# Optimization experiments

Measured on AMD Instinct MI355X. Metric: run time of the kernel, lower is better.

The kernel has to match this reference:

```python
import jax, jax.numpy as jnp
import numpy as np

B, T, IN, H, OUT = 64, 32, 256, 512, 256
M, W, R = 256, 64, 4            # nr_cells, cell_size, read_heads
NN_IN = IN + R * W              # 512
NN_OUT = H + R * W              # 768
IFACE = R * W + 3 * W + 5 * R + 3  # 471
CLIP = 20.0
DELTA = 1e-6


def setup_inputs():
    key = jax.random.key(0)
    ks = jax.random.split(key, 10)
    s = 0.05
    bound = float(np.sqrt(6.0 / (B * H + 2 * H)))  # xavier_uniform on (2,B,H)
    return {
        'x': jax.random.normal(ks[0], (B, T, IN), jnp.float32),
        'h0': jax.random.uniform(ks[1], (2, B, H), jnp.float32, -bound, bound),
        'Wih0': jax.random.normal(ks[2], (4 * H, NN_IN), jnp.float32) * s,
        'Whh0': jax.random.normal(ks[3], (4 * H, H), jnp.float32) * s,
        'bih0': jnp.zeros((4 * H,), jnp.float32),
        'bhh0': jnp.zeros((4 * H,), jnp.float32),
        'Wih1': jax.random.normal(ks[4], (4 * H, H), jnp.float32) * s,
        'Whh1': jax.random.normal(ks[5], (4 * H, H), jnp.float32) * s,
        'bih1': jnp.zeros((4 * H,), jnp.float32),
        'bhh1': jnp.zeros((4 * H,), jnp.float32),
        'Wif': jax.random.normal(ks[6], (IFACE, H), jnp.float32) * s,
        'bif': jnp.zeros((IFACE,), jnp.float32),
        'Wout': jax.random.normal(ks[7], (OUT, NN_OUT), jnp.float32) * s,
        'bout': jnp.zeros((OUT,), jnp.float32),
    }


def _lstm_cell(x, h, c, Wih, Whh, bih, bhh):
    g = x @ Wih.T + bih + h @ Whh.T + bhh
    i, f, gg, o = jnp.split(g, 4, axis=1)  # torch gate order i,f,g,o
    c = jax.nn.sigmoid(f) * c + jax.nn.sigmoid(i) * jnp.tanh(gg)
    h = jax.nn.sigmoid(o) * jnp.tanh(c)
    return h, c


def _content_weights(mem, keys, strengths):
    # mem: (b,M,W), keys: (b,K,W), strengths: (b,K) -> softmax over M
    mem_n = mem / (jnp.linalg.norm(mem, axis=2, keepdims=True) + DELTA)
    key_n = keys / (jnp.linalg.norm(keys, axis=2, keepdims=True) + DELTA)
    sim = jnp.einsum('bkw,bmw->bkm', key_n, mem_n)
    return jax.nn.softmax(sim * strengths[..., None], axis=2)


def _memory_step(xi, mem, link, prec, rw, ww, usage):
    b = xi.shape[0]
    o = 0
    rk = jnp.tanh(xi[:, :R * W].reshape(b, R, W)); o = R * W
    rs = jax.nn.softplus(xi[:, o:o + R]); o += R
    wk = jnp.tanh(xi[:, o:o + W]).reshape(b, 1, W); o += W
    ws = jax.nn.softplus(xi[:, o])[:, None]; o += 1
    ev = jax.nn.sigmoid(xi[:, o:o + W]); o += W
    wv = jnp.tanh(xi[:, o:o + W]); o += W
    fg = jax.nn.sigmoid(xi[:, o:o + R]); o += R
    ag = jax.nn.sigmoid(xi[:, o])[:, None]; o += 1
    wg = jax.nn.sigmoid(xi[:, o])[:, None]; o += 1
    rm = jax.nn.softmax(xi[:, o:o + 3 * R].reshape(b, R, 3), axis=2)

    # usage update (uses OLD read/write weights); single write head
    usage = usage + (1.0 - usage) * ww
    psi = jnp.prod(1.0 - fg[:, :, None] * rw, axis=1)
    usage = usage * psi

    # write content addressing on OLD memory
    wcw = _content_weights(mem, wk, ws)[:, 0]  # (b,M)

    # allocation by ascending sort of usage (exclusive cumprod)
    u = DELTA + (1.0 - DELTA) * usage
    phi = jnp.argsort(u, axis=1)
    sorted_u = jnp.take_along_axis(u, phi, axis=1)
    excl = jnp.cumprod(jnp.concatenate([jnp.ones((b, 1), u.dtype), sorted_u], axis=1), axis=1)[:, :-1]
    sorted_alloc = (1.0 - sorted_u) * excl
    alloc = jnp.take_along_axis(sorted_alloc, jnp.argsort(phi, axis=1), axis=1)

    ww = wg * (ag * alloc + (1.0 - ag) * wcw)  # (b,M)

    # erase + write
    mem = mem * (1.0 - ww[:, :, None] * ev[:, None, :]) + ww[:, :, None] * wv[:, None, :]

    # temporal link matrix + precedence
    prev_scale = 1.0 - ww[:, :, None] - ww[:, None, :]
    link = prev_scale * link + ww[:, :, None] * prec[:, None, :]
    link = link * (1.0 - jnp.eye(M, dtype=link.dtype))
    prec = (1.0 - ww.sum(axis=1, keepdims=True)) * prec + ww

    # read: directional weights use NEW link and OLD read weights; content uses NEW memory
    rcw = _content_weights(mem, rk, rs)               # (b,R,M)
    fwd = jnp.einsum('bij,brj->bri', link, rw)
    bwd = jnp.einsum('brj,bji->bri', rw, link)
    rw = rm[:, :, 0:1] * bwd + rm[:, :, 1:2] * fwd + rm[:, :, 2:3] * rcw
    rvec = jnp.einsum('brm,bmw->brw', rw, mem).reshape(b, R * W)
    return rvec, mem, link, prec, rw, ww, usage


def reference(x, h0, Wih0, Whh0, bih0, bhh0, Wih1, Whh1, bih1, bhh1, Wif, bif, Wout, bout):
    b = x.shape[0]
    lr0 = jnp.zeros((b, R * W), x.dtype)  # initial last_read; NOTE: source concatenates this
    # initial zero last_read to EVERY timestep's controller input (inputs built upfront)
    carry0 = (h0[0], h0[0], h0[1], h0[1],
              jnp.full((b, M, W), DELTA, x.dtype),   # memory
              jnp.zeros((b, M, M), x.dtype),          # link matrix
              jnp.zeros((b, M), x.dtype),             # precedence
              jnp.full((b, R, M), DELTA, x.dtype),    # read weights
              jnp.full((b, M), DELTA, x.dtype),       # write weights
              jnp.zeros((b, M), x.dtype))             # usage

    def step(carry, x_t):
        h0_, c0_, h1_, c1_, mem, link, prec, rw, ww, usage = carry
        inp = jnp.concatenate([x_t, lr0], axis=1)
        h0_, c0_ = _lstm_cell(inp, h0_, c0_, Wih0, Whh0, bih0, bhh0)
        h1_, c1_ = _lstm_cell(h0_, h1_, c1_, Wih1, Whh1, bih1, bhh1)
        out = jnp.clip(h1_, -CLIP, CLIP)
        xi = out @ Wif.T + bif
        rvec, mem, link, prec, rw, ww, usage = _memory_step(xi, mem, link, prec, rw, ww, usage)
        o_t = jnp.concatenate([out, rvec], axis=1)  # (b, NN_OUT)
        return (h0_, c0_, h1_, c1_, mem, link, prec, rw, ww, usage), o_t

    _, ys = jax.lax.scan(step, carry0, jnp.swapaxes(x, 0, 1))  # (T,b,NN_OUT)
    outputs = jnp.tanh(ys) @ Wout.T + bout  # Dropout(p=0) -> Tanh -> Linear
    return jnp.swapaxes(outputs, 0, 1)      # (b,T,OUT)
```

## Files before the change

kernel.cpp:

```cpp
#include <hip/hip_runtime.h>
#include <hip/hip_bf16.h>
#include <math.h>


typedef __bf16 bf16_t;
typedef __attribute__((ext_vector_type(8))) __bf16 bf16x8;
typedef __attribute__((ext_vector_type(4))) float f32x4;

#define B_    64
#define T_    32
#define IN_   256
#define H_    512
#define M_    256
#define W_    64
#define R_    4
#define IFACE_ 471
#define DELTA_ 1e-6f

#define OFF_H0SEQ  (0L)
#define SZ_H0SEQ   (32L*64*512*2)
#define OFF_OUTSEQ (OFF_H0SEQ + SZ_H0SEQ)
#define SZ_OUTSEQ  (32L*64*512*2)
#define OFF_H0BUF  (OFF_OUTSEQ + SZ_OUTSEQ)
#define SZ_HBUF    (2L*64*512*2)
#define OFF_H1BUF  (OFF_H0BUF + SZ_HBUF)
#define OFF_XI     (OFF_H1BUF + SZ_HBUF)
#define SZ_XI      (32L*64*480*4)
#define OFF_RVEC   (OFF_XI + SZ_XI)
#define SZ_RVEC    (32L*64*256*4)
#define OFF_YBF    (OFF_RVEC + SZ_RVEC)
#define SZ_YBF     (32L*64*768*2)
#define OFF_BAR    (OFF_YBF + SZ_YBF)
#define SZ_BAR     (256L)
#define OFF_XB     (OFF_BAR + SZ_BAR)
#define SZ_XB      (64L*32*256*2)
#define OFF_H0B    (OFF_XB + SZ_XB)
#define SZ_H0B     (2L*64*512*2)
#define OFF_W0     (OFF_H0B + SZ_H0B)
#define SZ_W       (2048L*512*2)
#define OFF_W1     (OFF_W0 + SZ_W)
#define OFF_W2     (OFF_W1 + SZ_W)
#define OFF_W3     (OFF_W2 + SZ_W)
#define OFF_WIF    (OFF_W3 + SZ_W)
#define SZ_WIF     (480L*512*2)
#define OFF_WOUTB  (OFF_WIF + SZ_WIF)
#define SZ_WOUTB   (256L*768*2)
#define OFF_BS0    (OFF_WOUTB + SZ_WOUTB)
#define SZ_BS      (2048L*4)
#define OFF_BS1    (OFF_BS0 + SZ_BS)
#define OFF_BIF    (OFF_BS1 + SZ_BS)
#define SZ_BIF     (2048L)
#define OFF_BOUTF  (OFF_BIF + SZ_BIF)
#define SZ_BOUTF   (1024L)
#define OFF_FLG    (OFF_BOUTF + SZ_BOUTF)
#define SZ_FLG     (4096L)

__device__ __forceinline__ float sigf(float x){ return 1.0f/(1.0f + expf(-x)); }
__device__ __forceinline__ float softplusf(float x){
  return fmaxf(x, 0.0f) + log1pf(expf(-fabsf(x)));
}
__device__ __forceinline__ float wred(float v){
  #pragma unroll
  for (int off = 32; off; off >>= 1) v += __shfl_xor(v, off, 64);
  return v;
}
__device__ __forceinline__ float ldin(const void* p, long i, int mf){
  return mf ? ((const float*)p)[i] : (float)((const bf16_t*)p)[i];
}

__device__ __forceinline__ void flagbar(unsigned* flg, int bid, unsigned tgt,
                                        int tid, int lane, int wv){
  __syncthreads();
  if (tid == 0)
    __hip_atomic_store(flg + (size_t)bid*16, tgt, __ATOMIC_RELEASE,
                       __HIP_MEMORY_SCOPE_AGENT);
  if (wv == 0){
    for (;;){
      unsigned f = __hip_atomic_load(flg + (size_t)lane*16, __ATOMIC_ACQUIRE,
                                     __HIP_MEMORY_SCOPE_AGENT);
      if (__all(f >= tgt)) break;
      __builtin_amdgcn_s_sleep(2);
    }
  }
  __syncthreads();
}

__global__ void k_detect(const unsigned short* __restrict__ x16,
                         int* __restrict__ flag, unsigned* __restrict__ bar,
                         unsigned* __restrict__ flg){
  __shared__ int cnt;
  if (threadIdx.x == 0){ cnt = 0; bar[0] = 0u; bar[1] = 0u; }
  for (int i = threadIdx.x; i < 1024; i += 256) flg[i] = 0u;
  __syncthreads();
  unsigned short u = x16[threadIdx.x * 2];
  int e = (u >> 7) & 0xFF;
  if (e >= 0x88) atomicAdd(&cnt, 1);
  __syncthreads();
  if (threadIdx.x == 0) *flag = (cnt > 16) ? 1 : 0;
}

__global__ void k_convert(const void* x, const void* h0, const void* Wih0,
                          const void* Whh0, const void* bih0, const void* bhh0,
                          const void* Wih1, const void* Whh1, const void* bih1,
                          const void* bhh1, const void* Wif, const void* bif,
                          const void* Wout, const void* bout,
                          bf16_t* __restrict__ xb, bf16_t* __restrict__ h0b,
                          bf16_t* __restrict__ h0buf, bf16_t* __restrict__ h1buf,
                          bf16_t* __restrict__ W0, bf16_t* __restrict__ W1,
                          bf16_t* __restrict__ W2, bf16_t* __restrict__ W3,
                          bf16_t* __restrict__ Wifp, bf16_t* __restrict__ Woutb,
                          float* __restrict__ bs0, float* __restrict__ bs1,
                          float* __restrict__ bifp, float* __restrict__ boutf,
                          const int* __restrict__ flag)
{
  const int mf = *flag;
  const long stride = (long)gridDim.x * blockDim.x;
  long i0 = (long)blockIdx.x * blockDim.x + threadIdx.x;
  switch (blockIdx.y){
  case 0: for (long i = i0; i < 64L*32*256; i += stride) xb[i] = (bf16_t)ldin(x, i, mf); break;
  case 1: for (long i = i0; i < 2L*64*512; i += stride){
            float v = ldin(h0, i, mf); bf16_t bb = (bf16_t)v; h0b[i] = bb;
            if (i < 64*512) h0buf[i] = bb; else h1buf[i - 64*512] = bb;
          } break;
  case 2: for (long i = i0; i < 2048L*512; i += stride) W0[i] = (bf16_t)ldin(Wih0, i, mf); break;
  case 3: for (long i = i0; i < 2048L*512; i += stride) W1[i] = (bf16_t)ldin(Whh0, i, mf); break;
  case 4: for (long i = i0; i < 2048L*512; i += stride) W2[i] = (bf16_t)ldin(Wih1, i, mf); break;
  case 5: for (long i = i0; i < 2048L*512; i += stride) W3[i] = (bf16_t)ldin(Whh1, i, mf); break;
  case 6: for (long i = i0; i < 480L*512; i += stride){
            long r = i >> 9;
            Wifp[i] = (r < IFACE_) ? (bf16_t)ldin(Wif, i, mf) : (bf16_t)0.0f;
          } break;
  case 7: for (long i = i0; i < 256L*768; i += stride) Woutb[i] = (bf16_t)ldin(Wout, i, mf); break;
  case 8:
    for (long i = i0; i < 2048; i += stride){
      bs0[i] = ldin(bih0, i, mf) + ldin(bhh0, i, mf);
      bs1[i] = ldin(bih1, i, mf) + ldin(bhh1, i, mf);
    }
    for (long i = i0; i < 480; i += stride) bifp[i] = (i < IFACE_) ? ldin(bif, i, mf) : 0.0f;
    for (long i = i0; i < 256; i += stride) boutf[i] = ldin(bout, i, mf);
    break;
  }
}

__device__ __forceinline__ void softmax256_wave(float* a, int lane){
  float v0=a[lane], v1=a[64+lane], v2=a[128+lane], v3=a[192+lane];
  float mx = fmaxf(fmaxf(v0,v1), fmaxf(v2,v3));
  #pragma unroll
  for (int off=32; off; off>>=1) mx = fmaxf(mx, __shfl_xor(mx, off, 64));
  v0=expf(v0-mx); v1=expf(v1-mx); v2=expf(v2-mx); v3=expf(v3-mx);
  float s = v0+v1+v2+v3;
  #pragma unroll
  for (int off=32; off; off>>=1) s += __shfl_xor(s, off, 64);
  float inv = 1.0f/s;
  a[lane]=v0*inv; a[64+lane]=v1*inv; a[128+lane]=v2*inv; a[192+lane]=v3*inv;
}

struct ProdShm {
  bf16_t wpool[66560];
  float  cst[64][16];
  float  bias[4][16];
};
struct ConsShm {
  float smem[256][65];
  float xib[480];
  float rkn4r[2][65][4];
  float wkn[64], ev_[64], wvv[64];
  float rs_[4], fg_[4], rm_[4][3];
  float wsS, agS, wgS, wwsumS;
  float invn[256], wcw[256];
  float usage[256], uu[256], su[256], scanA[256];
  int   rank_[256];
  float ww_[256], prec_[256];
  float rw_[4][256];
  float rw4[256][4];
  float fwd_[4][256], bwd_[4][256], rcw_[4][256];
  bf16_t rwb[4][264];
  bf16_t wwb[256], precb[256];
  float p2cT[2][264];
  float p5cT[5][2][264];
  float rvp[8][4][64];
};
union ShUnion { ProdShm p; ConsShm c; };

__global__ __launch_bounds__(512,2) void k_main(
    const bf16_t* __restrict__ xb, const bf16_t* __restrict__ h0b,
    const bf16_t* __restrict__ W0, const bf16_t* __restrict__ W1,
    const bf16_t* __restrict__ W2, const bf16_t* __restrict__ W3,
    const float* __restrict__ bs0, const float* __restrict__ bs1,
    const bf16_t* __restrict__ Wifp, const float* __restrict__ bifp,
    bf16_t* __restrict__ h0buf, bf16_t* __restrict__ h1buf,
    bf16_t* __restrict__ h0seq, bf16_t* __restrict__ outseq,
    float* __restrict__ XI, float* __restrict__ RVEC,
    unsigned* __restrict__ flg)
{
  __shared__ ShUnion sh;
  const int bid = blockIdx.x;
  const int tid = threadIdx.x, lane = tid & 63, wv = tid >> 6;
  const int m16 = lane & 15, q = lane >> 4;

  if (bid < 64){
    ProdShm& P = sh.p;
    const int layer = bid >> 5;
    const int u0 = (bid & 31) * 16;

    if (!layer){
      for (int i = tid; i < 64*32; i += 512){
        int rl = i >> 5, c8 = (i & 31)*8;
        int grow = (rl >> 4)*512 + u0 + (rl & 15);
        *(bf16x8*)&P.wpool[rl*264 + c8] = *(const bf16x8*)(W0 + (size_t)grow*512 + c8);
      }
      for (int i = tid; i < 64*64; i += 512){
        int rl = i >> 6, c8 = (i & 63)*8;
        int grow = (rl >> 4)*512 + u0 + (rl & 15);
        *(bf16x8*)&P.wpool[16896 + rl*520 + c8] = *(const bf16x8*)(W1 + (size_t)grow*512 + c8);
      }
    } else {
      for (int i = tid; i < 64*64; i += 512){
        int rl = i >> 6, c8 = (i & 63)*8;
        int grow = (rl >> 4)*512 + u0 + (rl & 15);
        *(bf16x8*)&P.wpool[rl*520 + c8]         = *(const bf16x8*)(W2 + (size_t)grow*512 + c8);
        *(bf16x8*)&P.wpool[33280 + rl*520 + c8] = *(const bf16x8*)(W3 + (size_t)grow*512 + c8);
      }
    }
    for (int i = tid; i < 64*16; i += 512){
      int b = i >> 4, n = i & 15;
      P.cst[b][n] = (float)h0b[layer*(64*512) + b*512 + u0 + n];
    }
    if (tid < 64){
      int G = tid >> 4, n = tid & 15;
      const float* bs = layer ? bs1 : bs0;
      P.bias[G][n] = bs[G*512 + u0 + n];
    }
    __syncthreads();

    bf16_t* hbuf = layer ? h1buf : h0buf;

    for (int ps = 0; ps <= 33; ++ps){
      if (wv < 4){
        const int t = layer ? (ps - 1) : ps;
        const bool active = layer ? (ps >= 1 && ps <= 32) : (ps < 32);
        if (active){
          const int p = t & 1;
          const bf16_t* hin = hbuf + p*(64*512);
          bf16_t* hout = hbuf + (p^1)*(64*512);
          const int b0 = wv * 16;

          f32x4 acc[4];
          #pragma unroll
          for (int G = 0; G < 4; ++G){ float bv = P.bias[G][m16]; acc[G] = (f32x4){bv,bv,bv,bv}; }

          if (!layer){
            #pragma unroll 2
            for (int kt = 0; kt < 8; ++kt){
              bf16x8 a = *(const bf16x8*)(xb + ((size_t)(b0+m16)*T_ + t)*IN_ + kt*32 + q*8);
              #pragma unroll
              for (int G = 0; G < 4; ++G)
                acc[G] = __builtin_amdgcn_mfma_f32_16x16x32_bf16(
                    a, *(const bf16x8*)&P.wpool[(G*16+m16)*264 + kt*32 + q*8], acc[G], 0, 0, 0);
            }
            #pragma unroll 4
            for (int kt = 0; kt < 16; ++kt){
              bf16x8 a = *(const bf16x8*)(hin + (b0+m16)*512 + kt*32 + q*8);
              #pragma unroll
              for (int G = 0; G < 4; ++G)
                acc[G] = __builtin_amdgcn_mfma_f32_16x16x32_bf16(
                    a, *(const bf16x8*)&P.wpool[16896 + (G*16+m16)*520 + kt*32 + q*8], acc[G], 0, 0, 0);
            }
          } else {
            #pragma unroll 4
            for (int kt = 0; kt < 16; ++kt){
              bf16x8 a = *(const bf16x8*)(h0seq + ((size_t)t*64 + b0+m16)*512 + kt*32 + q*8);
              #pragma unroll
              for (int G = 0; G < 4; ++G)
                acc[G] = __builtin_amdgcn_mfma_f32_16x16x32_bf16(
                    a, *(const bf16x8*)&P.wpool[(G*16+m16)*520 + kt*32 + q*8], acc[G], 0, 0, 0);
            }
            #pragma unroll 4
            for (int kt = 0; kt < 16; ++kt){
              bf16x8 a = *(const bf16x8*)(hin + (b0+m16)*512 + kt*32 + q*8);
              #pragma unroll
              for (int G = 0; G < 4; ++G)
                acc[G] = __builtin_amdgcn_mfma_f32_16x16x32_bf16(
                    a, *(const bf16x8*)&P.wpool[33280 + (G*16+m16)*520 + kt*32 + q*8], acc[G], 0, 0, 0);
            }
          }
          #pragma unroll
          for (int v = 0; v < 4; ++v){
            int b = b0 + q*4 + v;
            float gi = acc[0][v], gf = acc[1][v], gg = acc[2][v], go = acc[3][v];
            float c_ = sigf(gf)*P.cst[b][m16] + sigf(gi)*tanhf(gg);
            P.cst[b][m16] = c_;
            float h = sigf(go)*tanhf(c_);
            bf16_t hb = (bf16_t)h;
            hout[b*512 + u0 + m16] = hb;
            if (!layer) h0seq[((size_t)t*64 + b)*512 + u0 + m16] = hb;
            else        outseq[((size_t)t*64 + b)*512 + u0 + m16] = hb;
          }
        }
      } else if (ps >= 2 && bid < 30){
        const int t2 = ps - 2;
        const int b0 = (wv - 4) * 16;
        const int r = bid*16 + m16;
        float bv = bifp[r];
        f32x4 acc = {bv,bv,bv,bv};
        const bf16_t* arow = outseq + ((size_t)t2*64 + b0 + m16)*512 + q*8;
        const bf16_t* brow = Wifp + (size_t)r*512 + q*8;
        #pragma unroll 4
        for (int kt = 0; kt < 16; ++kt){
          acc = __builtin_amdgcn_mfma_f32_16x16x32_bf16(
              *(const bf16x8*)(arow + kt*32), *(const bf16x8*)(brow + kt*32), acc, 0, 0, 0);
        }
        #pragma unroll
        for (int v = 0; v < 4; ++v)
          XI[((size_t)t2*64 + b0 + q*4 + v)*480 + r] = acc[v];
      }
      flagbar(flg, bid, (unsigned)(ps + 1), tid, lane, wv);
    }
  } else {
    ConsShm& S = sh.c;
    const int b = bid - 64;
    const int quad = lane >> 4, li = lane & 15;

    bf16x8 rowL[2][8], colL[2][8];
    #pragma unroll
    for (int g = 0; g < 2; ++g)
      #pragma unroll
      for (int ch = 0; ch < 8; ++ch)
        #pragma unroll
        for (int z = 0; z < 8; ++z){ rowL[g][ch][z] = (bf16_t)0.0f; colL[g][ch][z] = (bf16_t)0.0f; }

    if (tid < 256){
      S.ww_[tid] = DELTA_; S.usage[tid] = 0.0f; S.prec_[tid] = 0.0f;
      S.invn[tid] = 1.0f/(sqrtf(64.0f*DELTA_*DELTA_) + DELTA_);
      S.wwb[tid] = (bf16_t)DELTA_; S.precb[tid] = (bf16_t)0.0f;
      #pragma unroll
      for (int r = 0; r < 4; ++r) S.rw_[r][tid] = DELTA_;
    }
    for (int i = tid; i < 4*264; i += 512) ((bf16_t*)S.rwb)[i] = (bf16_t)DELTA_;
    for (int i = tid; i < 256*65; i += 512) ((float*)S.smem)[i] = DELTA_;
    __syncthreads();

    const int mH = tid >> 1, q2 = tid & 1;

    for (int t = 0; t < 32; ++t){
      { const unsigned tgt = (unsigned)(t + 3);
        if (wv == 0){
          for (;;){
            unsigned f = __hip_atomic_load(flg + (size_t)lane*16, __ATOMIC_ACQUIRE,
                                           __HIP_MEMORY_SCOPE_AGENT);
            if (__all(f >= tgt)) break;
            __builtin_amdgcn_s_sleep(2);
          }
        }
        __syncthreads();
      }
      if (tid < IFACE_) S.xib[tid] = XI[((size_t)t*64 + b)*480 + tid];
      __syncthreads();

      if (wv < 4){
        float v = tanhf(S.xib[wv*64 + lane]);
        float s = wred(v*v);
        float vn = v/(sqrtf(s) + DELTA_);
        S.rkn4r[0][lane][wv] = vn; S.rkn4r[1][lane][wv] = vn;
      } else if (wv == 4){
        float v = tanhf(S.xib[260 + lane]);
        float s = wred(v*v);
        S.wkn[lane] = v/(sqrtf(s) + DELTA_);
      } else if (wv == 5){ S.ev_[lane] = sigf(S.xib[325 + lane]);
      } else if (wv == 6){ S.wvv[lane] = tanhf(S.xib[389 + lane]);
      } else {
        if (lane < 4)        S.rs_[lane] = softplusf(S.xib[256 + lane]);
        else if (lane == 4)  S.wsS = softplusf(S.xib[324]);
        else if (lane < 9)   S.fg_[lane-5] = sigf(S.xib[453 + (lane-5)]);
        else if (lane == 9)  S.agS = sigf(S.xib[457]);
        else if (lane == 10) S.wgS = sigf(S.xib[458]);
        else if (lane >= 16 && lane < 20){
          int r = lane - 16;
          float a0 = S.xib[459+r*3], a1 = S.xib[459+r*3+1], a2 = S.xib[459+r*3+2];
          float mx = fmaxf(a0, fmaxf(a1, a2));
          float e0 = expf(a0-mx), e1 = expf(a1-mx), e2 = expf(a2-mx);
          float s = e0+e1+e2;
          S.rm_[r][0]=e0/s; S.rm_[r][1]=e1/s; S.rm_[r][2]=e2/s;
        }
      }
      __syncthreads();

      if (tid < 256){
        int m = tid;
        float us = S.usage[m] + (1.0f - S.usage[m])*S.ww_[m];
        float psi = (1.0f - S.fg_[0]*S.rw_[0][m]) * (1.0f - S.fg_[1]*S.rw_[1][m])
                  * (1.0f - S.fg_[2]*S.rw_[2][m]) * (1.0f - S.fg_[3]*S.rw_[3][m]);
        us *= psi;
        S.usage[m] = us;
        S.uu[m] = DELTA_ + (1.0f - DELTA_)*us;
      }
      { float acc = 0.0f;
        #pragma unroll
        for (int it = 0; it < 32; ++it){
          int w = q2*32 + it;
          acc += S.smem[mH][w] * S.wkn[w];
        }
        S.p2cT[q2][mH] = acc; }
      __syncthreads();

      if (wv == 0){
        #pragma unroll
        for (int z = 0; z < 4; ++z){
          int m = z*64 + lane;
          S.wcw[m] = S.wsS * (S.p2cT[0][m] + S.p2cT[1][m]) * S.invn[m];
        }
        softmax256_wave(S.wcw, lane);
      } else if (tid >= 256){
        const int i = tid - 256;
        const float ui = S.uu[i];
        int cnt = 0;
        #pragma unroll 8
        for (int k = 0; k < 64; ++k){
          f32x4 u4 = *(const f32x4*)&S.uu[k*4];
          #pragma unroll
          for (int z = 0; z < 4; ++z){
            int j = k*4 + z; float uj = u4[z];
            cnt += (uj < ui || (uj == ui && j < i)) ? 1 : 0;
          }
        }
        S.rank_[i] = cnt;
        S.su[cnt] = ui;
      }
      __syncthreads();

      if (wv == 0){
        int base = lane*4;
        float v0 = S.su[base], v1 = S.su[base+1], v2 = S.su[base+2];
        float p1 = v0*v1, p2 = p1*v2, p3 = p2*S.su[base+3];
        float sc = p3;
        #pragma unroll
        for (int off = 1; off < 64; off <<= 1){
          float n = __shfl_up(sc, off, 64);
          if (lane >= off) sc *= n;
        }
        float exch = __shfl_up(sc, 1, 64);
        if (lane == 0) exch = 1.0f;
        S.scanA[base] = exch; S.scanA[base+1] = exch*v0;
        S.scanA[base+2] = exch*p1; S.scanA[base+3] = exch*p2;
      }
      __syncthreads();

      { const int m = mH;
        float al = (1.0f - S.uu[m]) * S.scanA[S.rank_[m]];
        float wm = S.wgS*(S.agS*al + (1.0f - S.agS)*S.wcw[m]);
        if (q2 == 0){ S.ww_[m] = wm; S.wwb[m] = (bf16_t)wm; }
        float s2 = 0.0f, sr0 = 0.0f, sr1 = 0.0f, sr2 = 0.0f, sr3 = 0.0f;
        #pragma unroll
        for (int it = 0; it < 32; ++it){
          int w = q2*32 + it;
          float mn = S.smem[m][w]*(1.0f - wm*S.ev_[w]) + wm*S.wvv[w];
          S.smem[m][w] = mn;
          s2 += mn*mn;
          f32x4 rk = *(const f32x4*)&S.rkn4r[q2][w][0];
          sr0 += mn*rk[0]; sr1 += mn*rk[1]; sr2 += mn*rk[2]; sr3 += mn*rk[3];
        }
        S.p5cT[0][q2][m] = s2;
        S.p5cT[1][q2][m] = sr0; S.p5cT[2][q2][m] = sr1;
        S.p5cT[3][q2][m] = sr2; S.p5cT[4][q2][m] = sr3; }
      __syncthreads();

      if (tid < 256){
        int m = tid;
        float s2 = S.p5cT[0][0][m] + S.p5cT[0][1][m];
        float inv = 1.0f/(sqrtf(s2) + DELTA_);
        S.invn[m] = inv;
        #pragma unroll
        for (int r = 0; r < 4; ++r){
          float sr = S.p5cT[r+1][0][m] + S.p5cT[r+1][1][m];
          S.rcw_[r][m] = S.rs_[r]*sr*inv;
        }
      } else if (wv == 4){
        float s = wred(S.ww_[lane] + S.ww_[64+lane] + S.ww_[128+lane] + S.ww_[192+lane]);
        if (lane == 0) S.wwsumS = s;
      }
      __syncthreads();

      { float wown[2], pown[2], alpha[2];
        #pragma unroll
        for (int g = 0; g < 2; ++g){
          int o = wv*32 + g*16 + li;
          wown[g] = (float)S.wwb[o]; pown[g] = (float)S.precb[o];
          alpha[g] = 1.0f - wown[g];
        }
        f32x4 facc[2] = {{0,0,0,0},{0,0,0,0}}, bacc[2] = {{0,0,0,0},{0,0,0,0}};
        #pragma unroll
        for (int ch = 0; ch < 8; ++ch){
          const int cbase = ch*32 + quad*8;
          bf16x8 rwf = *(const bf16x8*)&S.rwb[li & 3][cbase];
          bf16x8 wwv = *(const bf16x8*)&S.wwb[cbase];
          bf16x8 pcv = *(const bf16x8*)&S.precb[cbase];
          float wcf[8], pcf[8];
          #pragma unroll
          for (int jj = 0; jj < 8; ++jj){ wcf[jj] = (float)wwv[jj]; pcf[jj] = (float)pcv[jj]; }
          #pragma unroll
          for (int g = 0; g < 2; ++g){
            const int o = wv*32 + g*16 + li;
            bf16x8 rl = rowL[g][ch];
            bf16x8 cl = colL[g][ch];
            #pragma unroll
            for (int jj = 0; jj < 8; ++jj){
              const int c = cbase + jj;
              float s = alpha[g] - wcf[jj];
              float vr = s*(float)rl[jj] + wown[g]*pcf[jj];
              float vc = s*(float)cl[jj] + wcf[jj]*pown[g];
              if (c == o){ vr = 0.0f; vc = 0.0f; }
              rl[jj] = (bf16_t)vr;
              cl[jj] = (bf16_t)vc;
            }
            rowL[g][ch] = rl; colL[g][ch] = cl;
            facc[g] = __builtin_amdgcn_mfma_f32_16x16x32_bf16(rl, rwf, facc[g], 0, 0, 0);
            bacc[g] = __builtin_amdgcn_mfma_f32_16x16x32_bf16(rwf, cl, bacc[g], 0, 0, 0);
          }
        }
        #pragma unroll
        for (int g = 0; g < 2; ++g){
          if (li < 4){
            #pragma unroll
            for (int z = 0; z < 4; ++z) S.fwd_[li][wv*32 + g*16 + quad*4 + z] = facc[g][z];
          }
          if (quad == 0){
            #pragma unroll
            for (int z = 0; z < 4; ++z) S.bwd_[z][wv*32 + g*16 + li] = bacc[g][z];
          }
        }
      }
      __syncthreads();

      if (wv < 4) softmax256_wave(S.rcw_[wv], lane);
      else {
        int m = tid - 256;
        float p = (1.0f - S.wwsumS)*S.prec_[m] + S.ww_[m];
        S.prec_[m] = p;
        S.precb[m] = (bf16_t)p;
      }
      __syncthreads();

      { int r = tid >> 7, m0 = (tid & 127)*2;
        #pragma unroll
        for (int z = 0; z < 2; ++z){
          int m = m0 + z;
          float v = S.rm_[r][0]*S.bwd_[r][m] + S.rm_[r][1]*S.fwd_[r][m] + S.rm_[r][2]*S.rcw_[r][m];
          S.rw_[r][m] = v;
          S.rw4[m][r] = v;
          S.rwb[r][m] = (bf16_t)v;
        } }
      __syncthreads();

      { float r0 = 0, r1 = 0, r2 = 0, r3 = 0;
        #pragma unroll
        for (int k = 0; k < 32; ++k){
          int m = wv*32 + k;
          f32x4 r4 = *(const f32x4*)&S.rw4[m][0];
          float mv = S.smem[m][lane];
          r0 += r4[0]*mv; r1 += r4[1]*mv; r2 += r4[2]*mv; r3 += r4[3]*mv;
        }
        S.rvp[wv][0][lane] = r0; S.rvp[wv][1][lane] = r1;
        S.rvp[wv][2][lane] = r2; S.rvp[wv][3][lane] = r3; }
      __syncthreads();

      if (tid < 256){
        const int w = tid & 63, r = tid >> 6;
        float v = 0.0f;
        #pragma unroll
        for (int c = 0; c < 8; ++c) v += S.rvp[c][r][w];
        RVEC[((size_t)t*64 + b)*256 + tid] = v;
      }
      __syncthreads();
    }
  }
}

__global__ void k_tanhy(const bf16_t* __restrict__ outseq, const float* __restrict__ RVEC,
                        bf16_t* __restrict__ Y){
  const int n = 2048*768;
  for (int i = blockIdx.x*blockDim.x + threadIdx.x; i < n; i += gridDim.x*blockDim.x){
    int row = i / 768, j = i - row*768;
    float v = (j < 512) ? (float)outseq[(size_t)row*512 + j] : RVEC[(size_t)row*256 + (j - 512)];
    Y[i] = (bf16_t)tanhf(v);
  }
}

__global__ __launch_bounds__(256,1) void k_out(
    const bf16_t* __restrict__ Y, const bf16_t* __restrict__ Woutb,
    const float* __restrict__ boutf, void* __restrict__ dout,
    const int* __restrict__ flag)
{
  const int mf = *flag;
  const int mt = blockIdx.x;
  const int tid = threadIdx.x, lane = tid & 63, wv = tid >> 6;
  const int nt = blockIdx.y*4 + wv;
  const int m16 = lane & 15, q = lane >> 4;
  const int o = nt*16 + m16;
  float bv = boutf[o];
  f32x4 acc = {bv,bv,bv,bv};
  const bf16_t* arow = Y + (size_t)(mt*16 + m16)*768 + q*8;
  const bf16_t* brow = Woutb + (size_t)o*768 + q*8;
  for (int kt = 0; kt < 24; ++kt){
    acc = __builtin_amdgcn_mfma_f32_16x16x32_bf16(
        *(const bf16x8*)(arow + kt*32), *(const bf16x8*)(brow + kt*32), acc, 0, 0, 0);
  }
  #pragma unroll
  for (int v = 0; v < 4; ++v){
    int row = mt*16 + q*4 + v;
    int b = row & 63, t = row >> 6;
    size_t idx = ((size_t)b*T_ + t)*256 + o;
    if (mf) ((float*)dout)[idx] = acc[v];
    else    ((bf16_t*)dout)[idx] = (bf16_t)acc[v];
  }
}

extern "C" void kernel_launch(void* const* d_in, const int* in_sizes, int n_in,
                              void* d_out, int out_size, void* d_ws, size_t ws_size,
                              hipStream_t stream)
{
  char* ws = (char*)d_ws;
  bf16_t* H0SEQ  = (bf16_t*)(ws + OFF_H0SEQ);
  bf16_t* OUTSEQ = (bf16_t*)(ws + OFF_OUTSEQ);
  bf16_t* H0BUF  = (bf16_t*)(ws + OFF_H0BUF);
  bf16_t* H1BUF  = (bf16_t*)(ws + OFF_H1BUF);
  float*  XI     = (float*) (ws + OFF_XI);
  float*  RVEC   = (float*) (ws + OFF_RVEC);
  bf16_t* YBF    = (bf16_t*)(ws + OFF_YBF);
  unsigned* BAR  = (unsigned*)(ws + OFF_BAR);
  int*    FLAG   = (int*)   (ws + OFF_BAR + 8);
  bf16_t* XB     = (bf16_t*)(ws + OFF_XB);
  bf16_t* H0B    = (bf16_t*)(ws + OFF_H0B);
  bf16_t* W0     = (bf16_t*)(ws + OFF_W0);
  bf16_t* W1     = (bf16_t*)(ws + OFF_W1);
  bf16_t* W2     = (bf16_t*)(ws + OFF_W2);
  bf16_t* W3     = (bf16_t*)(ws + OFF_W3);
  bf16_t* WIFP   = (bf16_t*)(ws + OFF_WIF);
  bf16_t* WOUTB  = (bf16_t*)(ws + OFF_WOUTB);
  float*  BS0    = (float*) (ws + OFF_BS0);
  float*  BS1    = (float*) (ws + OFF_BS1);
  float*  BIFP   = (float*) (ws + OFF_BIF);
  float*  BOUTF  = (float*) (ws + OFF_BOUTF);
  unsigned* FLG  = (unsigned*)(ws + OFF_FLG);

  k_detect<<<1, 256, 0, stream>>>((const unsigned short*)d_in[0], FLAG, BAR, FLG);
  k_convert<<<dim3(256, 9), 256, 0, stream>>>(
      d_in[0], d_in[1], d_in[2], d_in[3], d_in[4], d_in[5], d_in[6],
      d_in[7], d_in[8], d_in[9], d_in[10], d_in[11], d_in[12], d_in[13],
      XB, H0B, H0BUF, H1BUF, W0, W1, W2, W3, WIFP, WOUTB,
      BS0, BS1, BIFP, BOUTF, FLAG);
  k_main<<<128, 512, 0, stream>>>(XB, H0B, W0, W1, W2, W3, BS0, BS1,
                                  WIFP, BIFP, H0BUF, H1BUF, H0SEQ, OUTSEQ,
                                  XI, RVEC, FLG);
  k_tanhy<<<512, 256, 0, stream>>>(OUTSEQ, RVEC, YBF);
  k_out<<<dim3(128, 4), 256, 0, stream>>>(YBF, WOUTB, BOUTF, d_out, FLAG);
}
```

Before: 1.135 ms.

## Use fast transcendental intrinsics, keep memory rows in registers, relax launch bounds

```diff
diff --git a/kernel.cpp b/kernel.cpp
--- a/kernel.cpp
+++ b/kernel.cpp
@@ -55,9 +55,16 @@
 #define OFF_FLG    (OFF_BOUTF + SZ_BOUTF)
 #define SZ_FLG     (4096L)
 
-__device__ __forceinline__ float sigf(float x){ return 1.0f/(1.0f + expf(-x)); }
+__device__ __forceinline__ float frcp(float x){ return __builtin_amdgcn_rcpf(x); }
+__device__ __forceinline__ float fsqrt_(float x){ return __builtin_amdgcn_sqrtf(x); }
+__device__ __forceinline__ float sigf(float x){ return frcp(1.0f + __expf(-x)); }
+__device__ __forceinline__ float tanh_f(float x){
+  float xc = fminf(fmaxf(x, -44.0f), 44.0f);
+  float t = __expf(2.0f * xc);
+  return (t - 1.0f) * frcp(t + 1.0f);
+}
 __device__ __forceinline__ float softplusf(float x){
-  return fmaxf(x, 0.0f) + log1pf(expf(-fabsf(x)));
+  return fmaxf(x, 0.0f) + __logf(1.0f + __expf(-fabsf(x)));
 }
 __device__ __forceinline__ float wred(float v){
   #pragma unroll
@@ -147,11 +154,11 @@
   float mx = fmaxf(fmaxf(v0,v1), fmaxf(v2,v3));
   #pragma unroll
   for (int off=32; off; off>>=1) mx = fmaxf(mx, __shfl_xor(mx, off, 64));
-  v0=expf(v0-mx); v1=expf(v1-mx); v2=expf(v2-mx); v3=expf(v3-mx);
+  v0=__expf(v0-mx); v1=__expf(v1-mx); v2=__expf(v2-mx); v3=__expf(v3-mx);
   float s = v0+v1+v2+v3;
   #pragma unroll
   for (int off=32; off; off>>=1) s += __shfl_xor(s, off, 64);
-  float inv = 1.0f/s;
+  float inv = frcp(s);
   a[lane]=v0*inv; a[64+lane]=v1*inv; a[128+lane]=v2*inv; a[192+lane]=v3*inv;
 }
 
@@ -182,7 +189,7 @@
 };
 union ShUnion { ProdShm p; ConsShm c; };
 
-__global__ __launch_bounds__(512,2) void k_main(
+__global__ __launch_bounds__(512) void k_main(
     const bf16_t* __restrict__ xb, const bf16_t* __restrict__ h0b,
     const bf16_t* __restrict__ W0, const bf16_t* __restrict__ W1,
     const bf16_t* __restrict__ W2, const bf16_t* __restrict__ W3,
@@ -288,9 +295,9 @@
           for (int v = 0; v < 4; ++v){
             int b = b0 + q*4 + v;
             float gi = acc[0][v], gf = acc[1][v], gg = acc[2][v], go = acc[3][v];
-            float c_ = sigf(gf)*P.cst[b][m16] + sigf(gi)*tanhf(gg);
+            float c_ = sigf(gf)*P.cst[b][m16] + sigf(gi)*tanh_f(gg);
             P.cst[b][m16] = c_;
-            float h = sigf(go)*tanhf(c_);
+            float h = sigf(go)*tanh_f(c_);
             bf16_t hb = (bf16_t)h;
             hout[b*512 + u0 + m16] = hb;
             if (!layer) h0seq[((size_t)t*64 + b)*512 + u0 + m16] = hb;
@@ -329,9 +336,13 @@
         #pragma unroll
         for (int z = 0; z < 8; ++z){ rowL[g][ch][z] = (bf16_t)0.0f; colL[g][ch][z] = (bf16_t)0.0f; }
 
+    float mr[32];
+    #pragma unroll
+    for (int z = 0; z < 32; ++z) mr[z] = DELTA_;
+
     if (tid < 256){
       S.ww_[tid] = DELTA_; S.usage[tid] = 0.0f; S.prec_[tid] = 0.0f;
-      S.invn[tid] = 1.0f/(sqrtf(64.0f*DELTA_*DELTA_) + DELTA_);
+      S.invn[tid] = 1.0f/(fsqrt_(64.0f*DELTA_*DELTA_) + DELTA_);
       S.wwb[tid] = (bf16_t)DELTA_; S.precb[tid] = (bf16_t)0.0f;
       #pragma unroll
       for (int r = 0; r < 4; ++r) S.rw_[r][tid] = DELTA_;
@@ -358,16 +369,16 @@
       __syncthreads();
 
       if (wv < 4){
-        float v = tanhf(S.xib[wv*64 + lane]);
+        float v = tanh_f(S.xib[wv*64 + lane]);
         float s = wred(v*v);
-        float vn = v/(sqrtf(s) + DELTA_);
+        float vn = v * frcp(fsqrt_(s) + DELTA_);
         S.rkn4r[0][lane][wv] = vn; S.rkn4r[1][lane][wv] = vn;
       } else if (wv == 4){
-        float v = tanhf(S.xib[260 + lane]);
+        float v = tanh_f(S.xib[260 + lane]);
         float s = wred(v*v);
-        S.wkn[lane] = v/(sqrtf(s) + DELTA_);
+        S.wkn[lane] = v * frcp(fsqrt_(s) + DELTA_);
       } else if (wv == 5){ S.ev_[lane] = sigf(S.xib[325 + lane]);
-      } else if (wv == 6){ S.wvv[lane] = tanhf(S.xib[389 + lane]);
+      } else if (wv == 6){ S.wvv[lane] = tanh_f(S.xib[389 + lane]);
       } else {
         if (lane < 4)        S.rs_[lane] = softplusf(S.xib[256 + lane]);
         else if (lane == 4)  S.wsS = softplusf(S.xib[324]);
@@ -378,9 +389,9 @@
           int r = lane - 16;
           float a0 = S.xib[459+r*3], a1 = S.xib[459+r*3+1], a2 = S.xib[459+r*3+2];
           float mx = fmaxf(a0, fmaxf(a1, a2));
-          float e0 = expf(a0-mx), e1 = expf(a1-mx), e2 = expf(a2-mx);
-          float s = e0+e1+e2;
-          S.rm_[r][0]=e0/s; S.rm_[r][1]=e1/s; S.rm_[r][2]=e2/s;
+          float e0 = __expf(a0-mx), e1 = __expf(a1-mx), e2 = __expf(a2-mx);
+          float inv = frcp(e0+e1+e2);
+          S.rm_[r][0]=e0*inv; S.rm_[r][1]=e1*inv; S.rm_[r][2]=e2*inv;
         }
       }
       __syncthreads();
@@ -398,7 +409,7 @@
         #pragma unroll
         for (int it = 0; it < 32; ++it){
           int w = q2*32 + it;
-          acc += S.smem[mH][w] * S.wkn[w];
+          acc += mr[it] * S.wkn[w];
         }
         S.p2cT[q2][mH] = acc; }
       __syncthreads();
@@ -453,7 +464,8 @@
         #pragma unroll
         for (int it = 0; it < 32; ++it){
           int w = q2*32 + it;
-          float mn = S.smem[m][w]*(1.0f - wm*S.ev_[w]) + wm*S.wvv[w];
+          float mn = mr[it]*(1.0f - wm*S.ev_[w]) + wm*S.wvv[w];
+          mr[it] = mn;
           S.smem[m][w] = mn;
           s2 += mn*mn;
           f32x4 rk = *(const f32x4*)&S.rkn4r[q2][w][0];
@@ -467,7 +479,7 @@
       if (tid < 256){
         int m = tid;
         float s2 = S.p5cT[0][0][m] + S.p5cT[0][1][m];
-        float inv = 1.0f/(sqrtf(s2) + DELTA_);
+        float inv = frcp(fsqrt_(s2) + DELTA_);
         S.invn[m] = inv;
         #pragma unroll
         for (int r = 0; r < 4; ++r){
@@ -581,7 +593,7 @@
   for (int i = blockIdx.x*blockDim.x + threadIdx.x; i < n; i += gridDim.x*blockDim.x){
     int row = i / 768, j = i - row*768;
     float v = (j < 512) ? (float)outseq[(size_t)row*512 + j] : RVEC[(size_t)row*256 + (j - 512)];
-    Y[i] = (bf16_t)tanhf(v);
+    Y[i] = (bf16_t)tanh_f(v);
   }
 }
 
```

New measurement: 1.082 ms. -4.7%, faster.
